# Performance work log

Measured on AMD Instinct MI355X. Metric: run time of the kernel, lower is better.

Reference implementation:

```python
import jax, jax.numpy as jnp
import numpy as np

N_BRANCH, N_LAYER = 4, 3
B, T, D_IN = 4, 1024, 32
D_MODEL, D_INNER, D_STATE, D_CONV, DT_RANK = 128, 256, 16, 4, 8
EMBED = 64
MAX_NORM = 10.0  # safe_expmap0 tangent-norm clip
EPS = 1e-7


def setup_inputs() -> dict:
    key = jax.random.key(0)
    ks = jax.random.split(key, 12)
    def nrm(k, shp, s=0.02):
        return s * jax.random.normal(k, shp, dtype=jnp.float32)
    A_init = jnp.log(jnp.arange(1, D_STATE + 1, dtype=jnp.float32))
    return {
        "trend": jax.random.normal(ks[0], (B, T, D_IN), jnp.float32),
        "seasonal_coarse": jax.random.normal(ks[1], (B, T, D_IN), jnp.float32),
        "seasonal_fine": jax.random.normal(ks[2], (B, T, D_IN), jnp.float32),
        "residual": jax.random.normal(ks[3], (B, T, D_IN), jnp.float32),
        "W_ip": nrm(ks[4], (N_BRANCH, D_IN, D_MODEL)),
        "b_ip": jnp.zeros((N_BRANCH, D_MODEL), jnp.float32),
        "W_in": nrm(ks[5], (N_BRANCH, N_LAYER, D_MODEL, 2 * D_INNER)),
        "conv_w": nrm(ks[6], (N_BRANCH, N_LAYER, D_INNER, D_CONV), 0.1),
        "conv_b": jnp.zeros((N_BRANCH, N_LAYER, D_INNER), jnp.float32),
        "W_x": nrm(ks[7], (N_BRANCH, N_LAYER, D_INNER, DT_RANK + 2 * D_STATE)),
        "W_dt": nrm(ks[8], (N_BRANCH, N_LAYER, DT_RANK, D_INNER), 0.1),
        "b_dt": jnp.full((N_BRANCH, N_LAYER, D_INNER), -4.6, jnp.float32),  # softplus ~ 0.01
        "A_log": jnp.broadcast_to(A_init, (N_BRANCH, N_LAYER, D_INNER, D_STATE)),
        "D_param": jnp.ones((N_BRANCH, N_LAYER, D_INNER), jnp.float32),
        "W_out": nrm(ks[9], (N_BRANCH, N_LAYER, D_INNER, D_MODEL)),
        "W_op": nrm(ks[10], (N_BRANCH, D_MODEL, EMBED)),
        "b_op": jnp.zeros((N_BRANCH, EMBED), jnp.float32),
        "eff_scale": jnp.asarray(0.1, jnp.float32),
    }


def _mamba_layer(x, Win, cw, cb, Wx, Wdt, bdt, Alog, Dp, Wout):
    # x: [B, T, d_model]
    Tlen = x.shape[1]
    xz = x @ Win                                   # [B,T,2*di]
    xp, z = jnp.split(xz, 2, axis=-1)
    # causal depthwise conv1d, kernel D_CONV
    xpad = jnp.pad(xp, ((0, 0), (D_CONV - 1, 0), (0, 0)))
    xc = sum(xpad[:, k:k + Tlen, :] * cw[:, k] for k in range(D_CONV))
    xc = jax.nn.silu(xc + cb)                      # [B,T,di]
    dbl = xc @ Wx                                  # [B,T,r+2s]
    dt = jax.nn.softplus(dbl[..., :DT_RANK] @ Wdt + bdt)   # [B,T,di]
    Bm = dbl[..., DT_RANK:DT_RANK + D_STATE]       # [B,T,s]
    Cm = dbl[..., DT_RANK + D_STATE:]              # [B,T,s]
    A = -jnp.exp(Alog)                             # [di,s]
    dA = jnp.exp(dt[..., None] * A)                # [B,T,di,s]
    dBx = (dt * xc)[..., None] * Bm[:, :, None, :] # [B,T,di,s]

    def step(h, inp):
        dA_t, dBx_t, C_t = inp
        h = dA_t * h + dBx_t
        return h, jnp.einsum('bds,bs->bd', h, C_t)

    h0 = jnp.zeros((x.shape[0], D_INNER, D_STATE), x.dtype)
    _, ys = jax.lax.scan(step, h0, (jnp.swapaxes(dA, 0, 1),
                                     jnp.swapaxes(dBx, 0, 1),
                                     jnp.swapaxes(Cm, 0, 1)))
    y = jnp.swapaxes(ys, 0, 1) + Dp * xc
    return (y * jax.nn.silu(z)) @ Wout


def _embed(x, Wip, bip, Wins, cws, cbs, Wxs, Wdts, bdts, Alogs, Dps, Wouts, Wop, bop):
    h = x @ Wip + bip
    for l in range(N_LAYER):
        h = _mamba_layer(h, Wins[l], cws[l], cbs[l], Wxs[l], Wdts[l], bdts[l],
                         Alogs[l], Dps[l], Wouts[l])
    return h.mean(axis=1) @ Wop + bop              # [B, EMBED]


def _expmap0(v):
    # safe expmap0 on Lorentz (k=1): clip tangent norm at MAX_NORM
    n = jnp.linalg.norm(v, axis=-1, keepdims=True)
    nc = jnp.clip(n, EPS, MAX_NORM)
    v = v * (nc / jnp.maximum(n, EPS))
    return jnp.concatenate([jnp.cosh(nc), jnp.sinh(nc) / nc * v], axis=-1)


def _projx(x):
    sp = x[..., 1:]
    t = jnp.sqrt(1.0 + jnp.sum(sp * sp, axis=-1, keepdims=True))
    return jnp.concatenate([t, sp], axis=-1)


def _logmap0(x):
    sp = x[..., 1:]
    t = jnp.maximum(x[..., :1], 1.0 + EPS)
    d = jnp.arccosh(t)
    spn = jnp.maximum(jnp.linalg.norm(sp, axis=-1, keepdims=True), EPS)
    return d * sp / spn


def _forward(trend, seasonal_coarse, seasonal_fine, residual,
             W_ip, b_ip, W_in, conv_w, conv_b, W_x, W_dt, b_dt,
             A_log, D_param, W_out, W_op, b_op, eff_scale):
    xs = [trend, seasonal_coarse, seasonal_fine, residual]
    z_t = [
        _embed(xs[b], W_ip[b], b_ip[b], W_in[b], conv_w[b], conv_b[b], W_x[b],
               W_dt[b], b_dt[b], A_log[b], D_param[b], W_out[b], W_op[b], b_op[b])
        for b in range(N_BRANCH)
    ]
    es = jnp.tanh(eff_scale)
    z_h = [_projx(_expmap0(z * es)) for z in z_t]
    us = [_logmap0(zh) for zh in z_h]
    combined_tangent = us[0] + us[1] + us[2] + us[3]
    combined_h = _projx(_expmap0(combined_tangent * es))
    return (*z_t, *z_h, combined_tangent, combined_h)


def reference(trend, seasonal_coarse, seasonal_fine, residual,
              W_ip, b_ip, W_in, conv_w, conv_b, W_x, W_dt, b_dt,
              A_log, D_param, W_out, W_op, b_op, eff_scale):
    return _forward(trend, seasonal_coarse, seasonal_fine, residual,
                    W_ip, b_ip, W_in, conv_w, conv_b, W_x, W_dt, b_dt,
                    A_log, D_param, W_out, W_op, b_op, eff_scale)
```

## Files before the change

kernel.cpp:

```cpp
#include <hip/hip_runtime.h>
#include <math.h>

#define NBR 4
#define NLAY 3
#define Bk 4
#define Tk 1024
#define DIN 32
#define DMODEL 128
#define DINNER 256
#define DSTATE 16
#define DTRANK 8
#define EMBEDk 64
#define BT (Bk*Tk)
#define EPSF 1e-7f
#define MAXNF 10.0f
#define LCH 64
#define NCH (Tk/LCH)
#define UF 8
#define NWB 320

typedef __bf16 bf16x8 __attribute__((ext_vector_type(8)));
typedef float  f32x4  __attribute__((ext_vector_type(4)));
typedef unsigned short u16x8 __attribute__((ext_vector_type(8)));

__device__ __forceinline__ float siluf(float x){ return x / (1.f + __expf(-x)); }
__device__ __forceinline__ float softplusf(float x){ return (x > 20.f) ? x : log1pf(__expf(x)); }
__device__ __forceinline__ unsigned short f2b(float x){
    union { float f; unsigned u; } v; v.f = x;
    unsigned r = v.u + 0x7FFF + ((v.u >> 16) & 1);
    return (unsigned short)(r >> 16);
}
__device__ __forceinline__ float b2f(unsigned short u){
    union { unsigned u; float f; } v; v.u = ((unsigned)u) << 16; return v.f;
}

__device__ __forceinline__ void gll16(const void* g, void* l){
    __builtin_amdgcn_global_load_lds(
        (const __attribute__((address_space(1))) unsigned int*)g,
        (__attribute__((address_space(3))) unsigned int*)l,
        16, 0, 0);
}

__device__ __forceinline__ void dA_pow(float q, float* dA){
    dA[0] = q;             dA[1] = q * q;
    dA[2] = dA[1] * dA[0]; dA[3] = dA[1] * dA[1];
    dA[4] = dA[3] * dA[0]; dA[5] = dA[3] * dA[1];
    dA[6] = dA[3] * dA[2]; dA[7] = dA[3] * dA[3];
    #pragma unroll
    for (int s = 8; s < 16; ++s) dA[s] = dA[s - 8] * dA[7];
}
__device__ __forceinline__ void dA_exp(float dtv, const float* Aa, float* dA){
    #pragma unroll
    for (int s = 0; s < 16; ++s) dA[s] = __expf(dtv * Aa[s]);
}

template<int MODE>
__global__ __launch_bounds__(256) void bgemm_k(
    const unsigned short* __restrict__ Ab, long aBr, int K,
    const unsigned short* __restrict__ Bt, long bBr,
    float* __restrict__ C0, long c0Br,
    float* __restrict__ C1, long c1Br,
    unsigned short* __restrict__ Cb, long cbBr,
    const float* __restrict__ bias, long biasBr)
{
    const int br = blockIdx.z;
    Ab += (long)br * aBr;
    Bt += (long)br * bBr;
    if (MODE == 3) C0 += (long)br * c0Br;
    if (MODE == 0 || MODE == 3) C1 += (long)br * c1Br;
    if (MODE == 0) Cb += (long)br * cbBr;
    if (MODE == 3) bias += (long)br * biasBr;
    const int m0 = blockIdx.x * 64, n0 = blockIdx.y * 64;
    __shared__ __align__(16) unsigned short As[8 * 64 * 8];
    __shared__ __align__(16) unsigned short Bs[8 * 64 * 8];
    const int tid = threadIdx.x;
    const int lane = tid & 63, w = tid >> 6;
    const int wm = w >> 1, wn = w & 1;
    const int quad = lane >> 4, l15 = lane & 15;
    f32x4 acc00 = {0,0,0,0}, acc01 = {0,0,0,0}, acc10 = {0,0,0,0}, acc11 = {0,0,0,0};
    for (int kc = 0; kc < K; kc += 64) {
        #pragma unroll
        for (int it = 0; it < 2; ++it) {
            const int kch = w + it * 4;
            gll16(Ab + (long)(m0 + lane) * K + kc + kch * 8, &As[(kch * 64) * 8]);
            gll16(Bt + (long)(n0 + lane) * K + kc + kch * 8, &Bs[(kch * 64) * 8]);
        }
        __syncthreads();
        #pragma unroll
        for (int k0 = 0; k0 < 64; k0 += 32) {
            const int kch = (k0 >> 3) + quad;
            bf16x8 a0 = *(const bf16x8*)&As[(kch * 64 + wm * 32 +      l15) * 8];
            bf16x8 a1 = *(const bf16x8*)&As[(kch * 64 + wm * 32 + 16 + l15) * 8];
            bf16x8 b0 = *(const bf16x8*)&Bs[(kch * 64 + wn * 32 +      l15) * 8];
            bf16x8 b1 = *(const bf16x8*)&Bs[(kch * 64 + wn * 32 + 16 + l15) * 8];
            acc00 = __builtin_amdgcn_mfma_f32_16x16x32_bf16(a0, b0, acc00, 0, 0, 0);
            acc01 = __builtin_amdgcn_mfma_f32_16x16x32_bf16(a0, b1, acc01, 0, 0, 0);
            acc10 = __builtin_amdgcn_mfma_f32_16x16x32_bf16(a1, b0, acc10, 0, 0, 0);
            acc11 = __builtin_amdgcn_mfma_f32_16x16x32_bf16(a1, b1, acc11, 0, 0, 0);
        }
        __syncthreads();
    }
    #pragma unroll
    for (int e = 0; e < 4; ++e) {
        f32x4 a = (e == 0) ? acc00 : (e == 1) ? acc01 : (e == 2) ? acc10 : acc11;
        const int msub = (e >> 1) * 16, nsub = (e & 1) * 16;
        const int col = n0 + wn * 32 + nsub + l15;
        #pragma unroll
        for (int r = 0; r < 4; ++r) {
            const int row = m0 + wm * 32 + msub + quad * 4 + r;
            const float v = a[r];
            if (MODE == 0) {
                if (n0 < 256) Cb[(long)row * 256 + col] = f2b(v);
                else          C1[(long)row * 256 + (col - 256)] = siluf(v);
            } else {
                if (col < 256)      C0[(long)row * 256 + col] = softplusf(v + bias[col]);
                else if (col < 288) C1[(long)row * 32 + (col - 256)] = v;
            }
        }
    }
}

__global__ __launch_bounds__(256) void prepT_k(
    const float* __restrict__ W, unsigned short* __restrict__ o,
    int Kd, int Nd, long wBr, long oBr)
{
    const int br = blockIdx.z;
    W += (long)br * wBr; o += (long)br * oBr;
    const int n0 = blockIdx.x * 64, k0 = blockIdx.y * 64;
    __shared__ float tile[64][65];
    const int t = threadIdx.x;
    #pragma unroll
    for (int i = 0; i < 16; ++i) {
        int idx = t + i * 256;
        int kl = idx >> 6, nl = idx & 63;
        tile[kl][nl] = W[(long)(k0 + kl) * Nd + n0 + nl];
    }
    __syncthreads();
    #pragma unroll
    for (int i = 0; i < 16; ++i) {
        int idx = t + i * 256;
        int nl = idx >> 6, kl = idx & 63;
        o[(long)(n0 + nl) * Kd + k0 + kl] = f2b(tile[kl][nl]);
    }
}

__global__ __launch_bounds__(256) void sgemmW_k(
    const float* __restrict__ Wout, const float* __restrict__ Win,
    float* __restrict__ Wtmp)
{
    const int z = blockIdx.z, p = z >> 2, br = z & 3;
    const float* A  = Wout + (long)(br * NLAY + p) * DINNER * DMODEL;
    const float* Bw = Win  + (long)(br * NLAY + p + 1) * DMODEL * 512;
    float* C = Wtmp + (long)z * DINNER * 512;
    const int m0 = blockIdx.x * 64, n0 = blockIdx.y * 64;
    __shared__ float As[32][68];
    __shared__ float Bs[32][68];
    const int tid = threadIdx.x;
    const int tx = tid & 15, ty = tid >> 4;
    float acc[4][4] = {};
    for (int kc = 0; kc < DMODEL; kc += 32) {
        #pragma unroll
        for (int it = 0; it < 2; ++it) {
            int id = tid + it * 256;
            int r = id >> 3, c4 = (id & 7) << 2;
            float4 v = *(const float4*)(A + (long)(m0 + r) * DMODEL + kc + c4);
            As[c4+0][r] = v.x; As[c4+1][r] = v.y; As[c4+2][r] = v.z; As[c4+3][r] = v.w;
            int rb = id >> 4, cb = (id & 15) << 2;
            *(float4*)&Bs[rb][cb] = *(const float4*)(Bw + (long)(kc + rb) * 512 + n0 + cb);
        }
        __syncthreads();
        #pragma unroll
        for (int kk = 0; kk < 32; ++kk) {
            float4 a4 = *(const float4*)&As[kk][ty << 2];
            float4 b4 = *(const float4*)&Bs[kk][tx << 2];
            float av[4] = {a4.x, a4.y, a4.z, a4.w};
            float bv[4] = {b4.x, b4.y, b4.z, b4.w};
            #pragma unroll
            for (int i = 0; i < 4; ++i)
                #pragma unroll
                for (int j = 0; j < 4; ++j)
                    acc[i][j] = fmaf(av[i], bv[j], acc[i][j]);
        }
        __syncthreads();
    }
    #pragma unroll
    for (int i = 0; i < 4; ++i) {
        int row = m0 + (ty << 2) + i, col = n0 + (tx << 2);
        float4 v4; v4.x = acc[i][0]; v4.y = acc[i][1]; v4.z = acc[i][2]; v4.w = acc[i][3];
        *(float4*)(C + (long)row * 512 + col) = v4;
    }
}

__global__ __launch_bounds__(256) void prepC_k(
    const float* __restrict__ Wx, const float* __restrict__ Wdt,
    unsigned short* __restrict__ o)
{
    const int n = blockIdx.x, bl = blockIdx.y;
    const int k = threadIdx.x;
    const float* WxP = Wx + (long)bl * DINNER * 40;
    float v;
    if (n < 256) {
        const float* WdtP = Wdt + (long)bl * DTRANK * DINNER;
        float s = 0.f;
        #pragma unroll
        for (int r = 0; r < 8; ++r) s = fmaf(WxP[k * 40 + r], WdtP[r * DINNER + n], s);
        v = s;
    } else if (n < 288) {
        v = WxP[k * 40 + 8 + (n - 256)];
    } else {
        v = 0.f;
    }
    o[(long)bl * NWB * DINNER + (long)n * DINNER + k] = f2b(v);
}

__global__ __launch_bounds__(256) void proj_k(
    const float* __restrict__ A0, const float* __restrict__ A1,
    const float* __restrict__ A2, const float* __restrict__ A3,
    const float* __restrict__ Bw, const float* __restrict__ bias,
    unsigned short* __restrict__ Cb)
{
    const int br = blockIdx.z;
    const float* A = (br == 1) ? A1 : (br == 2) ? A2 : (br == 3) ? A3 : A0;
    Bw   += (long)br * DIN * DMODEL;
    bias += (long)br * DMODEL;
    Cb   += (long)br * BT * DMODEL;
    const int m0 = blockIdx.x * 64, n0 = blockIdx.y * 64;
    __shared__ float As[32][68];
    __shared__ float Bs[32][68];
    const int tid = threadIdx.x;
    const int tx = tid & 15, ty = tid >> 4;
    float acc[4][4] = {};
    {
        #pragma unroll
        for (int it = 0; it < 2; ++it) {
            int id = tid + it * 256;
            int r = id >> 3, c4 = (id & 7) << 2;
            float4 v = *(const float4*)(A + (long)(m0 + r) * DIN + c4);
            As[c4+0][r] = v.x; As[c4+1][r] = v.y; As[c4+2][r] = v.z; As[c4+3][r] = v.w;
            int rb = id >> 4, cb = (id & 15) << 2;
            *(float4*)&Bs[rb][cb] = *(const float4*)(Bw + (long)rb * DMODEL + n0 + cb);
        }
        __syncthreads();
        #pragma unroll
        for (int kk = 0; kk < 32; ++kk) {
            float4 a4 = *(const float4*)&As[kk][ty << 2];
            float4 b4 = *(const float4*)&Bs[kk][tx << 2];
            float av[4] = {a4.x, a4.y, a4.z, a4.w};
            float bv[4] = {b4.x, b4.y, b4.z, b4.w};
            #pragma unroll
            for (int i = 0; i < 4; ++i)
                #pragma unroll
                for (int j = 0; j < 4; ++j)
                    acc[i][j] = fmaf(av[i], bv[j], acc[i][j]);
        }
    }
    const int col = n0 + (tx << 2);
    float bs[4];
    #pragma unroll
    for (int j = 0; j < 4; ++j) bs[j] = bias[col + j];
    #pragma unroll
    for (int i = 0; i < 4; ++i) {
        const int row = m0 + (ty << 2) + i;
        #pragma unroll
        for (int j = 0; j < 4; ++j)
            Cb[(long)row * DMODEL + col + j] = f2b(acc[i][j] + bs[j]);
    }
}

__global__ __launch_bounds__(256) void conv_k(
    const unsigned short* __restrict__ xp, const float* __restrict__ cw,
    const float* __restrict__ cb, unsigned short* __restrict__ xcb, int layer)
{
    const int br = blockIdx.y;
    const long base = (long)br * BT * DINNER;
    const long idx8 = ((long)blockIdx.x * 256 + threadIdx.x) * 8;
    const int d0 = (int)(idx8 & (DINNER - 1));
    const long row = idx8 >> 8;
    const int t = (int)(row & (Tk - 1));
    const float* cwp = cw + ((long)(br * NLAY + layer) * DINNER + d0) * 4;
    const float* cbp = cb + (long)(br * NLAY + layer) * DINNER + d0;
    u16x8 in[4];
    #pragma unroll
    for (int k = 0; k < 4; ++k) {
        const int tt = t + k - 3;
        if (tt >= 0) {
            in[k] = *(const u16x8*)(xp + base + idx8 + (long)(k - 3) * DINNER);
        } else {
            #pragma unroll
            for (int j = 0; j < 8; ++j) in[k][j] = 0;
        }
    }
    u16x8 o;
    #pragma unroll
    for (int j = 0; j < 8; ++j) {
        float acc = cbp[j];
        #pragma unroll
        for (int k = 0; k < 4; ++k)
            acc = fmaf(b2f(in[k][j]), cwp[j * 4 + k], acc);
        o[j] = f2b(siluf(acc));
    }
    *(u16x8*)(xcb + base + idx8) = o;
}

__global__ __launch_bounds__(256) void scan1_k(
    const float* __restrict__ dtb, const unsigned short* __restrict__ xcb,
    const float* __restrict__ bcb, const float* __restrict__ Alog,
    float* __restrict__ recbuf, int layer)
{
    const int c = blockIdx.x, b = blockIdx.y, br = blockIdx.z;
    const int d = threadIdx.x;
    const float* Ap = Alog + ((long)(br * NLAY + layer) * DINNER + d) * DSTATE;
    float Aa[16];
    bool pw = true;
    #pragma unroll
    for (int s = 0; s < 16; ++s) {
        Aa[s] = -__expf(Ap[s]);
        pw = pw && (fabsf(Aa[s] + (float)(s + 1)) < 1e-3f);
    }
    const long rbase = (long)br * BT + (long)b * Tk + (long)c * LCH;
    const float* dtp = dtb + rbase * DINNER + d;
    const unsigned short* xcp = xcb + rbase * DINNER + d;
    __shared__ float bcs[LCH * 32];
    {
        const float4* g = (const float4*)(bcb + rbase * 32);
        float4* l = (float4*)bcs;
        l[d] = g[d]; l[d + 256] = g[d + 256];
    }
    float dtc[UF], xcc[UF];
    #pragma unroll
    for (int u = 0; u < UF; ++u) {
        dtc[u] = dtp[(long)u * DINNER];
        xcc[u] = b2f(xcp[(long)u * DINNER]);
    }
    __syncthreads();
    float h[16];
    #pragma unroll
    for (int s = 0; s < 16; ++s) h[s] = 0.f;
    float sumdt = 0.f;
    for (int base = 0; base < LCH; base += UF) {
        const int nb = (base + UF < LCH) ? base + UF : base;
        float dtn[UF], xcn[UF];
        #pragma unroll
        for (int u = 0; u < UF; ++u) {
            dtn[u] = dtp[(long)(nb + u) * DINNER];
            xcn[u] = b2f(xcp[(long)(nb + u) * DINNER]);
        }
        #pragma unroll
        for (int u = 0; u < UF; ++u) {
            const int t = base + u;
            const float dtv = dtc[u];
            const float dtxc = dtv * xcc[u];
            sumdt += dtv;
            float dA[16];
            if (pw) dA_pow(__expf(-dtv), dA);
            else    dA_exp(dtv, Aa, dA);
            const float* bcT = bcs + t * 32;
            #pragma unroll
            for (int s = 0; s < 16; ++s)
                h[s] = fmaf(dA[s], h[s], dtxc * bcT[s]);
        }
        #pragma unroll
        for (int u = 0; u < UF; ++u) { dtc[u] = dtn[u]; xcc[u] = xcn[u]; }
    }
    float* sb = recbuf + (((long)(br * 4 + b) * (NCH - 1) + c) * 17) * 256 + d;
    #pragma unroll
    for (int s = 0; s < 16; ++s) sb[s * 256] = h[s];
    sb[16 * 256] = sumdt;
}

__global__ __launch_bounds__(256) void scan3_k(
    const float* __restrict__ dtb, const unsigned short* __restrict__ xcb,
    const float* __restrict__ bcb, const float* __restrict__ zb,
    const float* __restrict__ Alog, const float* __restrict__ Dpar,
    const float* __restrict__ recbuf, unsigned short* __restrict__ yzb, int layer)
{
    const int c = blockIdx.x, b = blockIdx.y, br = blockIdx.z;
    const int d = threadIdx.x;
    const float* Ap = Alog + ((long)(br * NLAY + layer) * DINNER + d) * DSTATE;
    float Aa[16];
    bool pw = true;
    #pragma unroll
    for (int s = 0; s < 16; ++s) {
        Aa[s] = -__expf(Ap[s]);
        pw = pw && (fabsf(Aa[s] + (float)(s + 1)) < 1e-3f);
    }
    float h[16];
    #pragma unroll
    for (int s = 0; s < 16; ++s) h[s] = 0.f;
    if (c > 0) {
        const float* recB = recbuf + ((long)(br * 4 + b) * (NCH - 1)) * 17 * 256 + d;
        float rh[16], rs;
        #pragma unroll
        for (int s = 0; s < 16; ++s) rh[s] = recB[s * 256];
        rs = recB[16 * 256];
        for (int cc = 0; cc < c; ++cc) {
            float nh[16], ns = 0.f;
            if (cc + 1 < c) {
                const float* r2 = recB + (long)(cc + 1) * 17 * 256;
                #pragma unroll
                for (int s = 0; s < 16; ++s) nh[s] = r2[s * 256];
                ns = r2[16 * 256];
            } else {
                #pragma unroll
                for (int s = 0; s < 16; ++s) nh[s] = 0.f;
            }
            float P[16];
            if (pw) dA_pow(__expf(-rs), P);
            else    dA_exp(rs, Aa, P);
            #pragma unroll
            for (int s = 0; s < 16; ++s) h[s] = fmaf(h[s], P[s], rh[s]);
            #pragma unroll
            for (int s = 0; s < 16; ++s) rh[s] = nh[s];
            rs = ns;
        }
    }
    const float Dp = Dpar[(br * NLAY + layer) * DINNER + d];
    const long rbase = (long)br * BT + (long)b * Tk + (long)c * LCH;
    const float* dtp = dtb + rbase * DINNER + d;
    const unsigned short* xcp = xcb + rbase * DINNER + d;
    const float* zp  = zb  + rbase * DINNER + d;
    unsigned short* yp = yzb + rbase * DINNER + d;
    __shared__ float bcs[LCH * 32];
    {
        const float4* g = (const float4*)(bcb + rbase * 32);
        float4* l = (float4*)bcs;
        l[d] = g[d]; l[d + 256] = g[d + 256];
    }
    float dtc[UF], xcc[UF], zc[UF];
    #pragma unroll
    for (int u = 0; u < UF; ++u) {
        dtc[u] = dtp[(long)u * DINNER];
        xcc[u] = b2f(xcp[(long)u * DINNER]);
        zc[u]  = zp[(long)u * DINNER];
    }
    __syncthreads();
    for (int base = 0; base < LCH; base += UF) {
        const int nb = (base + UF < LCH) ? base + UF : base;
        float dtn[UF], xcn[UF], zn[UF];
        #pragma unroll
        for (int u = 0; u < UF; ++u) {
            dtn[u] = dtp[(long)(nb + u) * DINNER];
            xcn[u] = b2f(xcp[(long)(nb + u) * DINNER]);
            zn[u]  = zp[(long)(nb + u) * DINNER];
        }
        #pragma unroll
        for (int u = 0; u < UF; ++u) {
            const int t = base + u;
            const float dtv = dtc[u], xcv = xcc[u];
            const float dtxc = dtv * xcv;
            float dA[16];
            if (pw) dA_pow(__expf(-dtv), dA);
            else    dA_exp(dtv, Aa, dA);
            const float* bcT = bcs + t * 32;
            #pragma unroll
            for (int s = 0; s < 16; ++s)
                h[s] = fmaf(dA[s], h[s], dtxc * bcT[s]);
            float y0 = 0.f, y1 = 0.f, y2 = 0.f, y3 = 0.f;
            #pragma unroll
            for (int s = 0; s < 16; s += 4) {
                y0 = fmaf(h[s+0], bcT[16+s+0], y0);
                y1 = fmaf(h[s+1], bcT[16+s+1], y1);
                y2 = fmaf(h[s+2], bcT[16+s+2], y2);
                y3 = fmaf(h[s+3], bcT[16+s+3], y3);
            }
            const float y = (y0 + y1) + (y2 + y3) + Dp * xcv;
            yp[(long)t * DINNER] = f2b(y * zc[u]);
        }
        #pragma unroll
        for (int u = 0; u < UF; ++u) { dtc[u] = dtn[u]; xcc[u] = xcn[u]; zc[u] = zn[u]; }
    }
}

__global__ __launch_bounds__(256) void csum1_k(
    const unsigned short* __restrict__ yz, float* __restrict__ part)
{
    const int ch = blockIdx.x, brb = blockIdx.y;
    const int br = brb >> 2, b = brb & 3;
    const long rbase = (long)br * BT + (long)b * Tk + (long)ch * 128;
    const int tid = threadIdx.x;
    const int cg = tid & 31;
    const int ro = tid >> 5;
    const unsigned short* p = yz + (rbase + ro) * DINNER + cg * 8;
    float acc[8] = {0,0,0,0,0,0,0,0};
    for (int it = 0; it < 16; ++it) {
        u16x8 v = *(const u16x8*)(p + (long)it * 8 * DINNER);
        #pragma unroll
        for (int j = 0; j < 8; ++j) acc[j] += b2f(v[j]);
    }
    __shared__ float sm[8][256];
    #pragma unroll
    for (int j = 0; j < 8; ++j) sm[ro][cg * 8 + j] = acc[j];
    __syncthreads();
    float s = 0.f;
    #pragma unroll
    for (int r = 0; r < 8; ++r) s += sm[r][tid];
    part[((long)brb * 8 + ch) * 256 + tid] = s;
}

__global__ __launch_bounds__(256) void csum2_k(
    const float* __restrict__ part, const float* __restrict__ Wout,
    const float* __restrict__ Wop, const float* __restrict__ bop,
    float* __restrict__ outzt)
{
    const int brb = blockIdx.x;
    const int br = brb >> 2, b = brb & 3;
    const int tid = threadIdx.x;
    __shared__ float v[256];
    __shared__ float u[128];
    float s = 0.f;
    #pragma unroll
    for (int ch = 0; ch < 8; ++ch) s += part[((long)brb * 8 + ch) * 256 + tid];
    v[tid] = s * (1.0f / Tk);
    __syncthreads();
    if (tid < 128) {
        const float* W2 = Wout + (long)(br * NLAY + 2) * DINNER * DMODEL;
        float a = 0.f;
        for (int k = 0; k < 256; ++k) a = fmaf(v[k], W2[k * DMODEL + tid], a);
        u[tid] = a;
    }
    __syncthreads();
    if (tid < EMBEDk) {
        float a = bop[br * EMBEDk + tid];
        for (int k = 0; k < 128; ++k)
            a = fmaf(u[k], Wop[(long)br * DMODEL * EMBEDk + k * EMBEDk + tid], a);
        outzt[br * (Bk * EMBEDk) + b * EMBEDk + tid] = a;
    }
}

__global__ __launch_bounds__(64) void final_k(
    const float* __restrict__ zt, float* __restrict__ out, const float* __restrict__ eff)
{
    const float es = tanhf(eff[0]);
    __shared__ float us[NBR][Bk][EMBEDk];
    const int t = threadIdx.x;
    if (t < 16) {
        const int br = t >> 2, b = t & 3;
        const float* z = zt + br * (Bk * EMBEDk) + b * EMBEDk;
        float n2 = 0.f;
        for (int e = 0; e < EMBEDk; ++e) { float v = z[e] * es; n2 = fmaf(v, v, n2); }
        const float n  = sqrtf(n2);
        const float nc = fminf(fmaxf(n, EPSF), MAXNF);
        const float sc = nc / fmaxf(n, EPSF);
        const float sh = sinhf(nc) / nc;
        const float fac = es * sc * sh;
        float* zh = out + 1024 + br * (Bk * (EMBEDk + 1)) + b * (EMBEDk + 1);
        float sp2 = 0.f;
        for (int e = 0; e < EMBEDk; ++e) {
            float spv = z[e] * fac;
            sp2 = fmaf(spv, spv, sp2);
            zh[1 + e] = spv;
            us[br][b][e] = spv;
        }
        const float t0 = sqrtf(1.f + sp2);
        zh[0] = t0;
        const float dd  = acoshf(fmaxf(t0, 1.f + EPSF));
        const float spn = fmaxf(sqrtf(sp2), EPSF);
        const float rr  = dd / spn;
        for (int e = 0; e < EMBEDk; ++e) us[br][b][e] *= rr;
    }
    __syncthreads();
    if (t < 4) {
        const int b = t;
        float ct[EMBEDk];
        float* cto = out + 2064 + b * EMBEDk;
        for (int e = 0; e < EMBEDk; ++e) {
            float v = us[0][b][e] + us[1][b][e] + us[2][b][e] + us[3][b][e];
            ct[e] = v; cto[e] = v;
        }
        float n2 = 0.f;
        for (int e = 0; e < EMBEDk; ++e) { float v = ct[e] * es; n2 = fmaf(v, v, n2); }
        const float n  = sqrtf(n2);
        const float nc = fminf(fmaxf(n, EPSF), MAXNF);
        const float sc = nc / fmaxf(n, EPSF);
        const float sh = sinhf(nc) / nc;
        const float fac = es * sc * sh;
        float* ch = out + 2320 + b * (EMBEDk + 1);
        float sp2 = 0.f;
        for (int e = 0; e < EMBEDk; ++e) {
            float spv = ct[e] * fac;
            sp2 = fmaf(spv, spv, sp2);
            ch[1 + e] = spv;
        }
        ch[0] = sqrtf(1.f + sp2);
    }
}

extern "C" void kernel_launch(void* const* d_in, const int* in_sizes, int n_in,
                              void* d_out, int out_size, void* d_ws, size_t ws_size,
                              hipStream_t stream)
{
    const float* X0 = (const float*)d_in[0];
    const float* X1 = (const float*)d_in[1];
    const float* X2 = (const float*)d_in[2];
    const float* X3 = (const float*)d_in[3];
    const float* W_ip   = (const float*)d_in[4];
    const float* b_ip   = (const float*)d_in[5];
    const float* W_in   = (const float*)d_in[6];
    const float* conv_w = (const float*)d_in[7];
    const float* conv_b = (const float*)d_in[8];
    const float* W_x    = (const float*)d_in[9];
    const float* W_dt   = (const float*)d_in[10];
    const float* b_dt   = (const float*)d_in[11];
    const float* A_log  = (const float*)d_in[12];
    const float* D_par  = (const float*)d_in[13];
    const float* W_out  = (const float*)d_in[14];
    const float* W_op   = (const float*)d_in[15];
    const float* b_op   = (const float*)d_in[16];
    const float* eff    = (const float*)d_in[17];
    float* out = (float*)d_out;
    float* ws  = (float*)d_ws;

    float* buf_z  = ws;
    float* buf_dt = buf_z  + (long)NBR * BT * DINNER;
    float* buf_bc = buf_dt + (long)NBR * BT * DINNER;
    float* part   = buf_bc + (long)NBR * BT * 32;
    float* recbuf = part   + (long)NBR * BT * DMODEL;
    float* Wtmp   = recbuf + (long)16 * (NCH - 1) * 17 * 256;
    unsigned short* h_bf  = (unsigned short*)(Wtmp + (long)8 * DINNER * 512);
    unsigned short* xp_bf = h_bf  + (long)NBR * BT * DMODEL;
    unsigned short* xc_bf = xp_bf + (long)NBR * BT * DINNER;
    unsigned short* yz_bf = xc_bf + (long)NBR * BT * DINNER;
    unsigned short* Win0T = yz_bf + (long)NBR * BT * DINNER;
    unsigned short* WfT   = Win0T + (long)NBR * 512 * DMODEL;
    unsigned short* WcT   = WfT   + (long)8 * 512 * DINNER;

    prepT_k<<<dim3(8, 2, NBR), 256, 0, stream>>>(
        W_in, Win0T, DMODEL, 512, (long)NLAY * DMODEL * 512, (long)512 * DMODEL);
    sgemmW_k<<<dim3(4, 8, 8), 256, 0, stream>>>(W_out, W_in, Wtmp);
    prepT_k<<<dim3(8, 4, 8), 256, 0, stream>>>(
        Wtmp, WfT, DINNER, 512, (long)DINNER * 512, (long)512 * DINNER);
    prepC_k<<<dim3(NWB, NBR * NLAY), 256, 0, stream>>>(W_x, W_dt, WcT);

    proj_k<<<dim3(BT / 64, DMODEL / 64, NBR), 256, 0, stream>>>(
        X0, X1, X2, X3, W_ip, b_ip, h_bf);

    for (int l = 0; l < NLAY; ++l) {
        if (l == 0) {
            bgemm_k<0><<<dim3(BT / 64, 8, NBR), 256, 0, stream>>>(
                h_bf, (long)BT * DMODEL, DMODEL,
                Win0T, (long)512 * DMODEL,
                nullptr, 0, buf_z, (long)BT * DINNER,
                xp_bf, (long)BT * DINNER, nullptr, 0);
        } else {
            bgemm_k<0><<<dim3(BT / 64, 8, NBR), 256, 0, stream>>>(
                yz_bf, (long)BT * DINNER, DINNER,
                WfT + (long)(l - 1) * 4 * 512 * DINNER, (long)512 * DINNER,
                nullptr, 0, buf_z, (long)BT * DINNER,
                xp_bf, (long)BT * DINNER, nullptr, 0);
        }
        conv_k<<<dim3((BT * DINNER) / (256 * 8), NBR), 256, 0, stream>>>(
            xp_bf, conv_w, conv_b, xc_bf, l);
        bgemm_k<3><<<dim3(BT / 64, NWB / 64, NBR), 256, 0, stream>>>(
            xc_bf, (long)BT * DINNER, DINNER,
            WcT + (long)l * NWB * DINNER, (long)NLAY * NWB * DINNER,
            buf_dt, (long)BT * DINNER, buf_bc, (long)BT * 32,
            nullptr, 0, b_dt + l * DINNER, (long)NLAY * DINNER);
        scan1_k<<<dim3(NCH - 1, Bk, NBR), 256, 0, stream>>>(
            buf_dt, xc_bf, buf_bc, A_log, recbuf, l);
        scan3_k<<<dim3(NCH, Bk, NBR), 256, 0, stream>>>(
            buf_dt, xc_bf, buf_bc, buf_z, A_log, D_par, recbuf, yz_bf, l);
    }

    csum1_k<<<dim3(8, 16), 256, 0, stream>>>(yz_bf, part);
    csum2_k<<<16, 256, 0, stream>>>(part, W_out, W_op, b_op, out);
    final_k<<<1, 64, 0, stream>>>(out, out, eff);
}
```

Measured before the change: 425.1 us.

## Fold input projection into first layer weights and fuse prep and tail kernels

Precomputes W_ip·W_in[0] plus the bias row as a combined 33x512 weight, so the first layer's in-projection runs directly from the raw 32-wide inputs. This drops the separate proj_k launch, the h_bf intermediate and the layer-0 bf16 GEMM. The transpose-to-bf16 step is folded into the weight-product kernel's epilogue, removing two prepT_k launches, and csum2 is merged with the final hyperbolic kernel. In exchange the combined first-layer product is computed in fp32 scalar FMA rather than MFMA, and the merged tail runs in a single block.

```diff
diff --git a/kernel.cpp b/kernel.cpp
--- a/kernel.cpp
+++ b/kernel.cpp
@@ -22,6 +22,7 @@
 typedef __bf16 bf16x8 __attribute__((ext_vector_type(8)));
 typedef float  f32x4  __attribute__((ext_vector_type(4)));
 typedef unsigned short u16x8 __attribute__((ext_vector_type(8)));
+typedef unsigned short u16x4 __attribute__((ext_vector_type(4)));
 
 __device__ __forceinline__ float siluf(float x){ return x / (1.f + __expf(-x)); }
 __device__ __forceinline__ float softplusf(float x){ return (x > 20.f) ? x : log1pf(__expf(x)); }
@@ -120,74 +121,100 @@
     }
 }
 
-__global__ __launch_bounds__(256) void prepT_k(
-    const float* __restrict__ W, unsigned short* __restrict__ o,
-    int Kd, int Nd, long wBr, long oBr)
-{
-    const int br = blockIdx.z;
-    W += (long)br * wBr; o += (long)br * oBr;
-    const int n0 = blockIdx.x * 64, k0 = blockIdx.y * 64;
-    __shared__ float tile[64][65];
-    const int t = threadIdx.x;
-    #pragma unroll
-    for (int i = 0; i < 16; ++i) {
-        int idx = t + i * 256;
-        int kl = idx >> 6, nl = idx & 63;
-        tile[kl][nl] = W[(long)(k0 + kl) * Nd + n0 + nl];
-    }
-    __syncthreads();
-    #pragma unroll
-    for (int i = 0; i < 16; ++i) {
-        int idx = t + i * 256;
-        int nl = idx >> 6, kl = idx & 63;
-        o[(long)(n0 + nl) * Kd + k0 + kl] = f2b(tile[kl][nl]);
-    }
-}
-
-__global__ __launch_bounds__(256) void sgemmW_k(
+__global__ __launch_bounds__(256) void sgemmWT_k(
     const float* __restrict__ Wout, const float* __restrict__ Win,
-    float* __restrict__ Wtmp)
-{
-    const int z = blockIdx.z, p = z >> 2, br = z & 3;
-    const float* A  = Wout + (long)(br * NLAY + p) * DINNER * DMODEL;
-    const float* Bw = Win  + (long)(br * NLAY + p + 1) * DMODEL * 512;
-    float* C = Wtmp + (long)z * DINNER * 512;
-    const int m0 = blockIdx.x * 64, n0 = blockIdx.y * 64;
-    __shared__ float As[32][68];
-    __shared__ float Bs[32][68];
+    const float* __restrict__ Wip, const float* __restrict__ bip,
+    unsigned short* __restrict__ WfT, float* __restrict__ Weq)
+{
+    const int z = blockIdx.z;
     const int tid = threadIdx.x;
     const int tx = tid & 15, ty = tid >> 4;
+    __shared__ float As_[32][68];
+    __shared__ float Bs_[32][68];
     float acc[4][4] = {};
-    for (int kc = 0; kc < DMODEL; kc += 32) {
-        #pragma unroll
-        for (int it = 0; it < 2; ++it) {
-            int id = tid + it * 256;
-            int r = id >> 3, c4 = (id & 7) << 2;
-            float4 v = *(const float4*)(A + (long)(m0 + r) * DMODEL + kc + c4);
-            As[c4+0][r] = v.x; As[c4+1][r] = v.y; As[c4+2][r] = v.z; As[c4+3][r] = v.w;
-            int rb = id >> 4, cb = (id & 15) << 2;
-            *(float4*)&Bs[rb][cb] = *(const float4*)(Bw + (long)(kc + rb) * 512 + n0 + cb);
-        }
-        __syncthreads();
-        #pragma unroll
-        for (int kk = 0; kk < 32; ++kk) {
-            float4 a4 = *(const float4*)&As[kk][ty << 2];
-            float4 b4 = *(const float4*)&Bs[kk][tx << 2];
-            float av[4] = {a4.x, a4.y, a4.z, a4.w};
-            float bv[4] = {b4.x, b4.y, b4.z, b4.w};
-            #pragma unroll
-            for (int i = 0; i < 4; ++i)
+    if (z < 8) {
+        const int p = z >> 2, br = z & 3;
+        const float* A  = Wout + (long)(br * NLAY + p) * DINNER * DMODEL;
+        const float* Bw = Win  + (long)(br * NLAY + p + 1) * DMODEL * 512;
+        const int m0 = blockIdx.x * 64, n0 = blockIdx.y * 64;
+        for (int kc = 0; kc < DMODEL; kc += 32) {
+            #pragma unroll
+            for (int it = 0; it < 2; ++it) {
+                int id = tid + it * 256;
+                int r = id >> 3, c4 = (id & 7) << 2;
+                float4 v = *(const float4*)(A + (long)(m0 + r) * DMODEL + kc + c4);
+                As_[c4+0][r] = v.x; As_[c4+1][r] = v.y; As_[c4+2][r] = v.z; As_[c4+3][r] = v.w;
+                int rb = id >> 4, cb = (id & 15) << 2;
+                *(float4*)&Bs_[rb][cb] = *(const float4*)(Bw + (long)(kc + rb) * 512 + n0 + cb);
+            }
+            __syncthreads();
+            #pragma unroll
+            for (int kk = 0; kk < 32; ++kk) {
+                float4 a4 = *(const float4*)&As_[kk][ty << 2];
+                float4 b4 = *(const float4*)&Bs_[kk][tx << 2];
+                float av[4] = {a4.x, a4.y, a4.z, a4.w};
+                float bv[4] = {b4.x, b4.y, b4.z, b4.w};
                 #pragma unroll
-                for (int j = 0; j < 4; ++j)
-                    acc[i][j] = fmaf(av[i], bv[j], acc[i][j]);
-        }
-        __syncthreads();
-    }
-    #pragma unroll
-    for (int i = 0; i < 4; ++i) {
-        int row = m0 + (ty << 2) + i, col = n0 + (tx << 2);
-        float4 v4; v4.x = acc[i][0]; v4.y = acc[i][1]; v4.z = acc[i][2]; v4.w = acc[i][3];
-        *(float4*)(C + (long)row * 512 + col) = v4;
+                for (int i = 0; i < 4; ++i)
+                    #pragma unroll
+                    for (int j = 0; j < 4; ++j)
+                        acc[i][j] = fmaf(av[i], bv[j], acc[i][j]);
+            }
+            __syncthreads();
+        }
+        unsigned short* o = WfT + (long)z * 512 * 256;
+        const int row0 = m0 + (ty << 2), col = n0 + (tx << 2);
+        #pragma unroll
+        for (int j = 0; j < 4; ++j) {
+            u16x4 v;
+            #pragma unroll
+            for (int i = 0; i < 4; ++i) v[i] = f2b(acc[i][j]);
+            *(u16x4*)(o + (long)(col + j) * 256 + row0) = v;
+        }
+    } else {
+        const int br = blockIdx.x;
+        const float* A  = Wip + (long)br * DIN * DMODEL;
+        const float* bp = bip + (long)br * DMODEL;
+        const float* Bw = Win + (long)br * NLAY * DMODEL * 512;
+        const int n0 = blockIdx.y * 64;
+        for (int kc = 0; kc < DMODEL; kc += 32) {
+            #pragma unroll
+            for (int it = 0; it < 2; ++it) {
+                int id = tid + it * 256;
+                int r = id >> 3, c4 = (id & 7) << 2;
+                float4 v;
+                if (r < 32)       v = *(const float4*)(A + (long)r * DMODEL + kc + c4);
+                else if (r == 32) v = *(const float4*)(bp + kc + c4);
+                else              { v.x = 0.f; v.y = 0.f; v.z = 0.f; v.w = 0.f; }
+                As_[c4+0][r] = v.x; As_[c4+1][r] = v.y; As_[c4+2][r] = v.z; As_[c4+3][r] = v.w;
+                int rb = id >> 4, cb = (id & 15) << 2;
+                *(float4*)&Bs_[rb][cb] = *(const float4*)(Bw + (long)(kc + rb) * 512 + n0 + cb);
+            }
+            __syncthreads();
+            #pragma unroll
+            for (int kk = 0; kk < 32; ++kk) {
+                float4 a4 = *(const float4*)&As_[kk][ty << 2];
+                float4 b4 = *(const float4*)&Bs_[kk][tx << 2];
+                float av[4] = {a4.x, a4.y, a4.z, a4.w};
+                float bv[4] = {b4.x, b4.y, b4.z, b4.w};
+                #pragma unroll
+                for (int i = 0; i < 4; ++i)
+                    #pragma unroll
+                    for (int j = 0; j < 4; ++j)
+                        acc[i][j] = fmaf(av[i], bv[j], acc[i][j]);
+            }
+            __syncthreads();
+        }
+        float* C = Weq + (long)br * 33 * 512;
+        const int col = n0 + (tx << 2);
+        #pragma unroll
+        for (int i = 0; i < 4; ++i) {
+            const int row = (ty << 2) + i;
+            if (row < 33) {
+                float4 v4; v4.x = acc[i][0]; v4.y = acc[i][1]; v4.z = acc[i][2]; v4.w = acc[i][3];
+                *(float4*)(C + (long)row * 512 + col) = v4;
+            }
+        }
     }
 }
 
@@ -213,20 +240,20 @@
     o[(long)bl * NWB * DINNER + (long)n * DINNER + k] = f2b(v);
 }
 
-__global__ __launch_bounds__(256) void proj_k(
+__global__ __launch_bounds__(256) void xgemm0_k(
     const float* __restrict__ A0, const float* __restrict__ A1,
     const float* __restrict__ A2, const float* __restrict__ A3,
-    const float* __restrict__ Bw, const float* __restrict__ bias,
-    unsigned short* __restrict__ Cb)
+    const float* __restrict__ Weq,
+    float* __restrict__ zb, unsigned short* __restrict__ xpb)
 {
     const int br = blockIdx.z;
     const float* A = (br == 1) ? A1 : (br == 2) ? A2 : (br == 3) ? A3 : A0;
-    Bw   += (long)br * DIN * DMODEL;
-    bias += (long)br * DMODEL;
-    Cb   += (long)br * BT * DMODEL;
+    const float* W = Weq + (long)br * 33 * 512;
+    float* C1 = zb + (long)br * BT * DINNER;
+    unsigned short* Cb = xpb + (long)br * BT * DINNER;
     const int m0 = blockIdx.x * 64, n0 = blockIdx.y * 64;
-    __shared__ float As[32][68];
-    __shared__ float Bs[32][68];
+    __shared__ float As_[32][68];
+    __shared__ float Bs_[32][68];
     const int tid = threadIdx.x;
     const int tx = tid & 15, ty = tid >> 4;
     float acc[4][4] = {};
@@ -236,15 +263,15 @@
             int id = tid + it * 256;
             int r = id >> 3, c4 = (id & 7) << 2;
             float4 v = *(const float4*)(A + (long)(m0 + r) * DIN + c4);
-            As[c4+0][r] = v.x; As[c4+1][r] = v.y; As[c4+2][r] = v.z; As[c4+3][r] = v.w;
+            As_[c4+0][r] = v.x; As_[c4+1][r] = v.y; As_[c4+2][r] = v.z; As_[c4+3][r] = v.w;
             int rb = id >> 4, cb = (id & 15) << 2;
-            *(float4*)&Bs[rb][cb] = *(const float4*)(Bw + (long)rb * DMODEL + n0 + cb);
+            *(float4*)&Bs_[rb][cb] = *(const float4*)(W + (long)rb * 512 + n0 + cb);
         }
         __syncthreads();
         #pragma unroll
         for (int kk = 0; kk < 32; ++kk) {
-            float4 a4 = *(const float4*)&As[kk][ty << 2];
-            float4 b4 = *(const float4*)&Bs[kk][tx << 2];
+            float4 a4 = *(const float4*)&As_[kk][ty << 2];
+            float4 b4 = *(const float4*)&Bs_[kk][tx << 2];
             float av[4] = {a4.x, a4.y, a4.z, a4.w};
             float bv[4] = {b4.x, b4.y, b4.z, b4.w};
             #pragma unroll
@@ -255,15 +282,18 @@
         }
     }
     const int col = n0 + (tx << 2);
-    float bs[4];
-    #pragma unroll
-    for (int j = 0; j < 4; ++j) bs[j] = bias[col + j];
+    float be[4];
+    #pragma unroll
+    for (int j = 0; j < 4; ++j) be[j] = W[32 * 512 + col + j];
     #pragma unroll
     for (int i = 0; i < 4; ++i) {
         const int row = m0 + (ty << 2) + i;
         #pragma unroll
-        for (int j = 0; j < 4; ++j)
-            Cb[(long)row * DMODEL + col + j] = f2b(acc[i][j] + bs[j]);
+        for (int j = 0; j < 4; ++j) {
+            const float v = acc[i][j] + be[j];
+            if (n0 < 256) Cb[(long)row * 256 + col + j] = f2b(v);
+            else          C1[(long)row * 256 + (col - 256 + j)] = siluf(v);
+        }
     }
 }
 
@@ -497,45 +527,51 @@
     part[((long)brb * 8 + ch) * 256 + tid] = s;
 }
 
-__global__ __launch_bounds__(256) void csum2_k(
+__global__ __launch_bounds__(256) void csum2f_k(
     const float* __restrict__ part, const float* __restrict__ Wout,
     const float* __restrict__ Wop, const float* __restrict__ bop,
-    float* __restrict__ outzt)
-{
-    const int brb = blockIdx.x;
-    const int br = brb >> 2, b = brb & 3;
+    const float* __restrict__ eff, float* __restrict__ out)
+{
     const int tid = threadIdx.x;
-    __shared__ float v[256];
-    __shared__ float u[128];
-    float s = 0.f;
-    #pragma unroll
-    for (int ch = 0; ch < 8; ++ch) s += part[((long)brb * 8 + ch) * 256 + tid];
-    v[tid] = s * (1.0f / Tk);
+    __shared__ float vm[16][256];
+    __shared__ float um[16][128];
+    __shared__ float zs[16][64];
+    __shared__ float us[NBR][Bk][EMBEDk];
+    #pragma unroll
+    for (int brb = 0; brb < 16; ++brb) {
+        float s = 0.f;
+        #pragma unroll
+        for (int chh = 0; chh < 8; ++chh) s += part[((long)brb * 8 + chh) * 256 + tid];
+        vm[brb][tid] = s * (1.0f / Tk);
+    }
     __syncthreads();
-    if (tid < 128) {
+    #pragma unroll
+    for (int i = 0; i < 8; ++i) {
+        const int idx = tid + i * 256;
+        const int brb = idx >> 7, colu = idx & 127;
+        const int br = brb >> 2;
         const float* W2 = Wout + (long)(br * NLAY + 2) * DINNER * DMODEL;
         float a = 0.f;
-        for (int k = 0; k < 256; ++k) a = fmaf(v[k], W2[k * DMODEL + tid], a);
-        u[tid] = a;
+        for (int k = 0; k < 256; ++k) a = fmaf(vm[brb][k], W2[k * DMODEL + colu], a);
+        um[brb][colu] = a;
     }
     __syncthreads();
-    if (tid < EMBEDk) {
-        float a = bop[br * EMBEDk + tid];
-        for (int k = 0; k < 128; ++k)
-            a = fmaf(u[k], Wop[(long)br * DMODEL * EMBEDk + k * EMBEDk + tid], a);
-        outzt[br * (Bk * EMBEDk) + b * EMBEDk + tid] = a;
-    }
-}
-
-__global__ __launch_bounds__(64) void final_k(
-    const float* __restrict__ zt, float* __restrict__ out, const float* __restrict__ eff)
-{
+    #pragma unroll
+    for (int i = 0; i < 4; ++i) {
+        const int idx = tid + i * 256;
+        const int brb = idx >> 6, e = idx & 63;
+        const int br = brb >> 2;
+        float a = bop[br * EMBEDk + e];
+        for (int k = 0; k < DMODEL; ++k)
+            a = fmaf(um[brb][k], Wop[(long)br * DMODEL * EMBEDk + k * EMBEDk + e], a);
+        zs[brb][e] = a;
+        out[brb * EMBEDk + e] = a;
+    }
+    __syncthreads();
     const float es = tanhf(eff[0]);
-    __shared__ float us[NBR][Bk][EMBEDk];
-    const int t = threadIdx.x;
-    if (t < 16) {
-        const int br = t >> 2, b = t & 3;
-        const float* z = zt + br * (Bk * EMBEDk) + b * EMBEDk;
+    if (tid < 16) {
+        const int br = tid >> 2, b = tid & 3;
+        const float* z = zs[br * 4 + b];
         float n2 = 0.f;
         for (int e = 0; e < EMBEDk; ++e) { float v = z[e] * es; n2 = fmaf(v, v, n2); }
         const float n  = sqrtf(n2);
@@ -559,8 +595,8 @@
         for (int e = 0; e < EMBEDk; ++e) us[br][b][e] *= rr;
     }
     __syncthreads();
-    if (t < 4) {
-        const int b = t;
+    if (tid < 4) {
+        const int b = tid;
         float ct[EMBEDk];
         float* cto = out + 2064 + b * EMBEDk;
         for (int e = 0; e < EMBEDk; ++e) {
@@ -574,14 +610,14 @@
         const float sc = nc / fmaxf(n, EPSF);
         const float sh = sinhf(nc) / nc;
         const float fac = es * sc * sh;
-        float* ch = out + 2320 + b * (EMBEDk + 1);
+        float* chh = out + 2320 + b * (EMBEDk + 1);
         float sp2 = 0.f;
         for (int e = 0; e < EMBEDk; ++e) {
             float spv = ct[e] * fac;
             sp2 = fmaf(spv, spv, sp2);
-            ch[1 + e] = spv;
-        }
-        ch[0] = sqrtf(1.f + sp2);
+            chh[1 + e] = spv;
+        }
+        chh[0] = sqrtf(1.f + sp2);
     }
 }
 
@@ -614,34 +650,22 @@
     float* buf_dt = buf_z  + (long)NBR * BT * DINNER;
     float* buf_bc = buf_dt + (long)NBR * BT * DINNER;
     float* part   = buf_bc + (long)NBR * BT * 32;
-    float* recbuf = part   + (long)NBR * BT * DMODEL;
-    float* Wtmp   = recbuf + (long)16 * (NCH - 1) * 17 * 256;
-    unsigned short* h_bf  = (unsigned short*)(Wtmp + (long)8 * DINNER * 512);
-    unsigned short* xp_bf = h_bf  + (long)NBR * BT * DMODEL;
+    float* recbuf = part   + 32768;
+    float* Weq    = recbuf + (long)16 * (NCH - 1) * 17 * 256;
+    unsigned short* xp_bf = (unsigned short*)(Weq + 4 * 33 * 512);
     unsigned short* xc_bf = xp_bf + (long)NBR * BT * DINNER;
     unsigned short* yz_bf = xc_bf + (long)NBR * BT * DINNER;
-    unsigned short* Win0T = yz_bf + (long)NBR * BT * DINNER;
-    unsigned short* WfT   = Win0T + (long)NBR * 512 * DMODEL;
+    unsigned short* WfT   = yz_bf + (long)NBR * BT * DINNER;
     unsigned short* WcT   = WfT   + (long)8 * 512 * DINNER;
 
-    prepT_k<<<dim3(8, 2, NBR), 256, 0, stream>>>(
-        W_in, Win0T, DMODEL, 512, (long)NLAY * DMODEL * 512, (long)512 * DMODEL);
-    sgemmW_k<<<dim3(4, 8, 8), 256, 0, stream>>>(W_out, W_in, Wtmp);
-    prepT_k<<<dim3(8, 4, 8), 256, 0, stream>>>(
-        Wtmp, WfT, DINNER, 512, (long)DINNER * 512, (long)512 * DINNER);
     prepC_k<<<dim3(NWB, NBR * NLAY), 256, 0, stream>>>(W_x, W_dt, WcT);
-
-    proj_k<<<dim3(BT / 64, DMODEL / 64, NBR), 256, 0, stream>>>(
-        X0, X1, X2, X3, W_ip, b_ip, h_bf);
+    sgemmWT_k<<<dim3(4, 8, 9), 256, 0, stream>>>(W_out, W_in, W_ip, b_ip, WfT, Weq);
+
+    xgemm0_k<<<dim3(BT / 64, 8, NBR), 256, 0, stream>>>(
+        X0, X1, X2, X3, Weq, buf_z, xp_bf);
 
     for (int l = 0; l < NLAY; ++l) {
-        if (l == 0) {
-            bgemm_k<0><<<dim3(BT / 64, 8, NBR), 256, 0, stream>>>(
-                h_bf, (long)BT * DMODEL, DMODEL,
-                Win0T, (long)512 * DMODEL,
-                nullptr, 0, buf_z, (long)BT * DINNER,
-                xp_bf, (long)BT * DINNER, nullptr, 0);
-        } else {
+        if (l > 0) {
             bgemm_k<0><<<dim3(BT / 64, 8, NBR), 256, 0, stream>>>(
                 yz_bf, (long)BT * DINNER, DINNER,
                 WfT + (long)(l - 1) * 4 * 512 * DINNER, (long)512 * DINNER,
@@ -662,6 +686,5 @@
     }
 
     csum1_k<<<dim3(8, 16), 256, 0, stream>>>(yz_bf, part);
-    csum2_k<<<16, 256, 0, stream>>>(part, W_out, W_op, b_op, out);
-    final_k<<<1, 64, 0, stream>>>(out, out, eff);
-}
+    csum2f_k<<<1, 256, 0, stream>>>(part, W_out, W_op, b_op, eff, out);
+}
```

New measurement: 474.6 us. 1.12x slower.
